# Performance work log

Hardware: AMD Instinct MI355X
Metric: run time of the kernel (lower is better)

The kernel has to match this reference:

```python
import jax, jax.numpy as jnp
import numpy as np

T, B, L, D = 32, 128, 1024, 256  # timesteps, batch, memory slots, word_vec_size(=rnn_size)


def setup_inputs() -> dict:
    key = jax.random.key(0)
    ks = jax.random.split(key, 20)
    f = lambda k, s: jax.random.normal(k, s, dtype=jnp.float32) * 0.05
    return {
        "emb_utts": f(ks[0], (T, B, D)),
        "hr0": f(ks[1], (B, D)),
        "cr0": f(ks[2], (B, D)),
        "hw0": f(ks[3], (B, D)),
        "cw0": f(ks[4], (B, D)),
        "M": f(ks[5], (B, L, D)),
        "mask": jax.random.randint(ks[6], (B, L), 0, 2).astype(bool),
        "Wih_r": f(ks[7], (4 * D, D)),
        "Whh_r": f(ks[8], (4 * D, D)),
        "bih_r": f(ks[9], (4 * D,)),
        "bhh_r": f(ks[10], (4 * D,)),
        "Wc": f(ks[11], (D, 2 * D)),
        "bc": f(ks[12], (D,)),
        "Wih_w": f(ks[13], (4 * D, D)),
        "Whh_w": f(ks[14], (4 * D, D)),
        "bih_w": f(ks[15], (4 * D,)),
        "bhh_w": f(ks[16], (4 * D,)),
    }


def _lstm_cell(x, h, c, Wih, Whh, bih, bhh):
    # PyTorch LSTMCell gate order: i, f, g, o
    g = x @ Wih.T + h @ Whh.T + bih + bhh
    i, fg, gg, o = jnp.split(g, 4, axis=1)
    i = jax.nn.sigmoid(i)
    fg = jax.nn.sigmoid(fg)
    gg = jnp.tanh(gg)
    o = jax.nn.sigmoid(o)
    c2 = fg * c + i * gg
    return o * jnp.tanh(c2), c2


def reference(emb_utts, hr0, cr0, hw0, cw0, M, mask,
              Wih_r, Whh_r, bih_r, bhh_r, Wc, bc,
              Wih_w, Whh_w, bih_w, bhh_w):
    def step(carry, w):
        hr, cr, hw, cw, Mc = carry
        hr, cr = _lstm_cell(w, hr, cr, Wih_r, Whh_r, bih_r, bhh_r)
        # attention read: z = softmax(masked(hr . M))  -> [B, L]
        z = jnp.einsum('bd,bld->bl', hr, Mc)
        z = jax.nn.softmax(jnp.where(mask, -jnp.inf, z), axis=1)
        m = jnp.einsum('bl,bld->bd', z, Mc)           # gather read [B, D]
        comp = jax.nn.softmax(jnp.concatenate([hr, m], axis=1) @ Wc.T + bc, axis=1)
        hw, cw = _lstm_cell(comp, hw, cw, Wih_w, Whh_w, bih_w, bhh_w)
        # memory rewrite exactly as source: M_new = (1 - z) + hw * z (broadcast)
        Mc = (1.0 - z[:, :, None]) + hw[:, None, :] * z[:, :, None]
        return (hr, cr, hw, cw, Mc), hw

    (hr, cr, hw, cw, M), outputs = jax.lax.scan(
        step, (hr0, cr0, hw0, cw0, M), emb_utts)
    return outputs, hr, cr, hw, cw, M
```

## Files before the change

### kernel.cpp

```cpp
#include <hip/hip_runtime.h>
#include <math.h>

typedef unsigned int u32;
typedef __attribute__((ext_vector_type(2))) _Float16 h2;

#define kT 32
#define OUT_STATES 1048576
#define OUT_M      1179648

union H2U { u32 u; h2 h; };

__device__ __forceinline__ float dot2u(u32 w, u32 x, float acc){
  H2U a; a.u = w; H2U b; b.u = x;
#if __has_builtin(__builtin_amdgcn_fdot2)
  return __builtin_amdgcn_fdot2(a.h, b.h, acc, false);
#else
  acc += (float)a.h.x * (float)b.h.x;
  acc += (float)a.h.y * (float)b.h.y;
  return acc;
#endif
}

__device__ __forceinline__ u32 packf16(float x, float y){
  H2U v; v.h.x = (_Float16)x; v.h.y = (_Float16)y; return v.u;
}

__device__ __forceinline__ u32 alu(const u32* p){
  return __hip_atomic_load((u32*)p, __ATOMIC_RELAXED, __HIP_MEMORY_SCOPE_AGENT);
}
__device__ __forceinline__ float alf(const float* p){
  return __hip_atomic_load((float*)p, __ATOMIC_RELAXED, __HIP_MEMORY_SCOPE_AGENT);
}
__device__ __forceinline__ void asu(u32* p, u32 v){
  __hip_atomic_store(p, v, __ATOMIC_RELAXED, __HIP_MEMORY_SCOPE_AGENT);
}
__device__ __forceinline__ void asf(float* p, float v){
  __hip_atomic_store(p, v, __ATOMIC_RELAXED, __HIP_MEMORY_SCOPE_AGENT);
}

__device__ __forceinline__ void pollk(const u32* f, int n, u32 tgt, int tid){
  if (tid < 64){
    const u32* p = f + ((tid < n) ? tid : 0);
    for (;;){
      if (__all((int)(alu(p) >= tgt))) break;
      __builtin_amdgcn_s_sleep(2);
    }
  }
  __syncthreads();
}

__global__ __launch_bounds__(1024) void k_prep(
        const float* __restrict__ Wih_r, const float* __restrict__ Whh_r,
        const float* __restrict__ bih_r, const float* __restrict__ bhh_r,
        const float* __restrict__ Wc,    const float* __restrict__ bc,
        const float* __restrict__ Wih_w, const float* __restrict__ Whh_w,
        const float* __restrict__ bih_w, const float* __restrict__ bhh_w,
        const unsigned char* __restrict__ maskraw,
        u32* WAp, u32* WEp, u32* Wcp, float* bA, float* bE, float* bcf,
        float* wcs, unsigned char* mbuf, u32* flags){
  __shared__ int sb[3];
  if (threadIdx.x < 3) sb[threadIdx.x] = 0;
  __syncthreads();
  if (threadIdx.x < 512){
    unsigned char c = maskraw[threadIdx.x];
    if (c > 1u) atomicOr(&sb[0], 1);
    if ((threadIdx.x & 3) != 0 && c != 0) atomicOr(&sb[1], 1);
    if ((threadIdx.x & 3) == 1 && c == 0x3F) atomicOr(&sb[2], 1);
  }
  __syncthreads();
  int mode = (!sb[0]) ? (sb[1] ? 1 : 0) : (sb[2] ? 2 : 3);

  int idx = blockIdx.x * 1024 + threadIdx.x;
  if (idx < 262144){
    int col = idx >> 8, kp = idx & 255;
    int k0 = 2 * kp;
    float v0 = (k0 < 256) ? Wih_r[col * 256 + k0] : Whh_r[col * 256 + k0 - 256];
    float v1 = (k0 < 256) ? Wih_r[col * 256 + k0 + 1]
                          : Whh_r[col * 256 + k0 + 1 - 256];
    WAp[kp * 1024 + col] = packf16(v0, v1);
  } else if (idx < 524288){
    int i = idx - 262144;
    int col = i >> 8, kp = i & 255;
    int k0 = 2 * kp;
    float v0 = (k0 < 256) ? Wih_w[col * 256 + k0] : Whh_w[col * 256 + k0 - 256];
    float v1 = (k0 < 256) ? Wih_w[col * 256 + k0 + 1]
                          : Whh_w[col * 256 + k0 + 1 - 256];
    WEp[kp * 1024 + col] = packf16(v0, v1);
  } else if (idx < 589824){
    int i = idx - 524288;
    int col = i >> 8, kp = i & 255;
    Wcp[kp * 256 + col] = packf16(Wc[col * 512 + 2 * kp], Wc[col * 512 + 2 * kp + 1]);
  } else if (idx < 590848){
    int i = idx - 589824;
    bA[i] = bih_r[i] + bhh_r[i];
  } else if (idx < 591872){
    int i = idx - 590848;
    bE[i] = bih_w[i] + bhh_w[i];
  } else if (idx < 592128){
    int i = idx - 591872;
    bcf[i] = bc[i];
  } else if (idx < 592384){
    int c = idx - 592128;
    float s = 0.f;
    for (int k = 0; k < 256; k++) s += Wc[c * 512 + 256 + k];
    wcs[c] = s;
  } else if (idx < 723456){
    int l = idx - 592384;
    unsigned char mv;
    if      (mode == 0) mv = (((const int*)maskraw)[l] != 0);
    else if (mode == 1) mv = (maskraw[l] != 0);
    else if (mode == 2) mv = ((maskraw[2*l] | maskraw[2*l+1]) != 0);
    else                mv = (((const unsigned int*)maskraw)[l] != 0);
    mbuf[l] = mv;
  } else if (idx < 724224){
    flags[idx - 723456] = 0;
  }
}

__global__ __launch_bounds__(1024) void k_pre(
        const float* __restrict__ emb, const u32* __restrict__ WAp,
        u32* __restrict__ gxp){
  __shared__ u32 wt[16384];
  __shared__ u32 xt[128 * 129];
  int t = blockIdx.x, c0 = blockIdx.y * 128, tid = threadIdx.x;
  for (int i = 0; i < 16; i++){
    int idx = i * 1024 + tid;
    wt[idx] = WAp[(size_t)(idx >> 7) * 1024 + c0 + (idx & 127)];
    int b = idx >> 7, kp = idx & 127;
    float2 e2 = *(const float2*)(emb + (size_t)t * 32768 + b * 256 + 2 * kp);
    xt[b * 129 + kp] = packf16(e2.x, e2.y);
  }
  __syncthreads();
  int b = tid & 127, cg = tid >> 7;
  float acc[16];
  #pragma unroll
  for (int j = 0; j < 16; j++) acc[j] = 0.f;
  const u32* xrow = xt + b * 129;
  for (int kp = 0; kp < 128; kp++){
    u32 xv = xrow[kp];
    const uint4* wr = (const uint4*)(wt + kp * 128 + cg * 16);
    #pragma unroll
    for (int j4 = 0; j4 < 4; j4++){
      uint4 wv = wr[j4];
      acc[4*j4+0] = dot2u(wv.x, xv, acc[4*j4+0]);
      acc[4*j4+1] = dot2u(wv.y, xv, acc[4*j4+1]);
      acc[4*j4+2] = dot2u(wv.z, xv, acc[4*j4+2]);
      acc[4*j4+3] = dot2u(wv.w, xv, acc[4*j4+3]);
    }
  }
  u32* gp = gxp + ((size_t)t * 128 + b) * 512 + (c0 >> 1) + cg * 8;
  #pragma unroll
  for (int i = 0; i < 8; i++) gp[i] = packf16(acc[2*i], acc[2*i+1]);
}

__device__ __forceinline__ void gemv256(const u32* __restrict__ W,
        const u32* xh, float* psum, int tid){
  int cg = tid & 255, ks = tid >> 8;
  const uint4* wp = (const uint4*)W + (size_t)ks * 32 * 256 + cg;
  const u32* xk = xh + ks * 32;
  float a0 = 0.f, a1 = 0.f, a2 = 0.f, a3 = 0.f;
  #pragma unroll 8
  for (int i = 0; i < 32; i++){
    uint4 wv = wp[(size_t)i * 256];
    u32 xp = xk[i];
    a0 = dot2u(wv.x, xp, a0);  a1 = dot2u(wv.y, xp, a1);
    a2 = dot2u(wv.z, xp, a2);  a3 = dot2u(wv.w, xp, a3);
  }
  float4 r; r.x = a0; r.y = a1; r.z = a2; r.w = a3;
  *(float4*)&psum[ks * 1024 + cg * 4] = r;
}

__device__ __forceinline__ void gemv128x256(const u32* __restrict__ W,
        const u32* xh, float* psum, int tid){
  int c = tid & 255, ks = tid >> 8;
  const u32* wp = W + (size_t)(ks * 32) * 256 + c;
  const u32* xk = xh + ks * 32;
  float a = 0.f;
  #pragma unroll 8
  for (int i = 0; i < 32; i++) a = dot2u(wp[(size_t)i * 256], xk[i], a);
  psum[ks * 256 + c] = a;
}

__device__ void scan_half(int k, const float* __restrict__ M0,
        const unsigned char* __restrict__ mbuf, const float* __restrict__ hrf,
        float* spbuf, float* mpbuf, float* msbuf, u32* fT0, const u32* fR,
        char* sc, int tid){
  float* ps   = (float*)(sc);
  float* wred = (float*)(sc + 16640);
  float* sred = (float*)(sc + 16704);
  float* hr0l = (float*)(sc + 16768);
  int row = k >> 1, half = k & 1;
  pollk(fR + row, 1, 1u, tid);
  if (tid < 256) hr0l[tid] = alf(hrf + row * 256 + tid);
  __syncthreads();
  int w = tid >> 6, lane = tid & 63;
  float4 hrv = *(const float4*)&hr0l[lane * 4];
  float run_max = -INFINITY, S = 0.f;
  float m0 = 0.f, m1 = 0.f, m2 = 0.f, m3 = 0.f;
  int l0 = half * 512 + w * 32;
  for (int l = l0; l < l0 + 32; ++l){
    float4 Mv = *(const float4*)(M0 + ((size_t)row * 1024 + l) * 256 + lane * 4);
    float part = Mv.x * hrv.x + Mv.y * hrv.y + Mv.z * hrv.z + Mv.w * hrv.w;
    #pragma unroll
    for (int mm = 32; mm >= 1; mm >>= 1) part += __shfl_xor(part, mm, 64);
    float s = mbuf[row * 1024 + l] ? -INFINITY : part;
    if (lane == 0) asf(spbuf + row * 1024 + l, s);
    float nm = fmaxf(run_max, s);
    if (nm > -INFINITY){
      float sc2 = expf(run_max - nm);
      float p   = expf(s - nm);
      S = S * sc2 + p;
      m0 = m0 * sc2 + p * Mv.x;  m1 = m1 * sc2 + p * Mv.y;
      m2 = m2 * sc2 + p * Mv.z;  m3 = m3 * sc2 + p * Mv.w;
      run_max = nm;
    }
  }
  if (lane == 0){ wred[w] = run_max; sred[w] = S; }
  ps[w * 260 + lane * 4 + 0] = m0;
  ps[w * 260 + lane * 4 + 1] = m1;
  ps[w * 260 + lane * 4 + 2] = m2;
  ps[w * 260 + lane * 4 + 3] = m3;
  __syncthreads();
  float gmax = -INFINITY;
  #pragma unroll
  for (int w2 = 0; w2 < 16; w2++) gmax = fmaxf(gmax, wred[w2]);
  float Sg = 0.f;
  #pragma unroll
  for (int w2 = 0; w2 < 16; w2++) Sg += sred[w2] * expf(wred[w2] - gmax);
  if (tid < 256){
    float mv = 0.f;
    #pragma unroll
    for (int w2 = 0; w2 < 16; w2++) mv += ps[w2 * 260 + tid] * expf(wred[w2] - gmax);
    asf(mpbuf + k * 256 + tid, mv);
  }
  if (tid == 0){ asf(msbuf + 2 * k, gmax); asf(msbuf + 2 * k + 1, Sg); }
  __syncthreads();
  if (tid == 0) asu(fT0 + k, 1u);
}

__global__ __launch_bounds__(1024, 4) void k_main(
        const float* __restrict__ hr0, const float* __restrict__ cr0,
        const float* __restrict__ hw0, const float* __restrict__ cw0,
        const float* __restrict__ M0,
        const u32* __restrict__ WAp, const u32* __restrict__ WEp,
        const u32* __restrict__ Wcp, const float* __restrict__ bA,
        const float* __restrict__ bE, const float* __restrict__ bcf,
        const float* __restrict__ wcs, const unsigned char* __restrict__ mbuf,
        const u32* __restrict__ gxp,
        float* __restrict__ hrf, float* __restrict__ ubuf,
        float* __restrict__ gwbuf,
        u32* __restrict__ hwp, float* __restrict__ zsbuf,
        float* __restrict__ hwfin, float* __restrict__ spbuf,
        float* __restrict__ mpbuf, float* __restrict__ msbuf,
        u32* __restrict__ flags, float* __restrict__ out){
  __shared__ __attribute__((aligned(16))) char smem[86016];
  int bid = blockIdx.x, tid = threadIdx.x;
  int w = tid >> 6, lane = tid & 63;
  u32* fR  = flags;
  u32* fG  = flags + 192;
  u32* fW  = flags + 256;
  u32* fT0 = flags + 320;

  if (bid < 128){
    int b = bid;
    float* psum = (float*)(smem);
    u32*  xh    = (u32*)(smem + 16384);
    float* hr_f = (float*)(smem + 16896);
    const u32* WRh = WAp + 128 * 1024;
    float cst = (tid < 256) ? cr0[b * 256 + tid] : 0.f;
    if (tid < 128){
      float2 h0 = *(const float2*)(hr0 + b * 256 + 2 * tid);
      xh[tid] = packf16(h0.x, h0.y);
    }
    __syncthreads();
    for (int t = 0; t < kT; t++){
      if (t >= 2) pollk(fW + (b >> 1), 1, (u32)(t - 1), tid);
      u32 gx0 = 0, gx1 = 0, gx2 = 0, gx3 = 0;
      if (tid < 256){
        const u32* gx = gxp + ((size_t)t * 128 + b) * 512;
        gx0 = gx[tid >> 1];          gx1 = gx[128 + (tid >> 1)];
        gx2 = gx[256 + (tid >> 1)];  gx3 = gx[384 + (tid >> 1)];
      }
      gemv256(WRh, xh, psum, tid);
      __syncthreads();
      if (tid < 256){
        H2U p0, p1, p2, p3;
        p0.u = gx0; p1.u = gx1; p2.u = gx2; p3.u = gx3;
        int hi = tid & 1;
        float gi = (hi ? (float)p0.h.y : (float)p0.h.x) + bA[tid];
        float gf = (hi ? (float)p1.h.y : (float)p1.h.x) + bA[256 + tid];
        float gg = (hi ? (float)p2.h.y : (float)p2.h.x) + bA[512 + tid];
        float go = (hi ? (float)p3.h.y : (float)p3.h.x) + bA[768 + tid];
        #pragma unroll
        for (int ks = 0; ks < 4; ks++){
          gi += psum[ks * 1024 + tid];
          gf += psum[ks * 1024 + 256 + tid];
          gg += psum[ks * 1024 + 512 + tid];
          go += psum[ks * 1024 + 768 + tid];
        }
        float i_ = 1.f / (1.f + expf(-gi));
        float f_ = 1.f / (1.f + expf(-gf));
        float g_ = tanhf(gg);
        float o_ = 1.f / (1.f + expf(-go));
        float c2 = f_ * cst + i_ * g_;
        cst = c2;
        float h = o_ * tanhf(c2);
        hr_f[tid] = h;
        asf(hrf + (t & 1) * 32768 + b * 256 + tid, h);
        if (t == kT - 1){
          out[OUT_STATES          + b * 256 + tid] = h;
          out[OUT_STATES +  32768 + b * 256 + tid] = c2;
        }
      }
      __syncthreads();
      if (tid < 128) xh[tid] = packf16(hr_f[2 * tid], hr_f[2 * tid + 1]);
      __syncthreads();
      gemv128x256(Wcp, xh, psum, tid);
      __syncthreads();
      if (tid < 256){
        float u = psum[tid] + psum[256 + tid] + psum[512 + tid] + psum[768 + tid];
        asf(ubuf + (t & 1) * 32768 + b * 256 + tid, u);
      }
      __syncthreads();
      if (tid == 0) asu(fR + b, (u32)(t + 1));
      if (t == 0)
        scan_half(bid, M0, mbuf, hrf, spbuf, mpbuf, msbuf, fT0, fR,
                  smem + 49152, tid);
    }
  } else if (bid < 192){
    int g = bid - 128, r0 = 2 * g, r1 = 2 * g + 1;
    float* psum = (float*)(smem);
    u32*  xh    = (u32*)(smem + 32768);
    for (int t = 0; t < kT; t++){
      if (t == 0){
        if (tid < 128){
          float2 h0 = *(const float2*)(hw0 + r0 * 256 + 2 * tid);
          xh[tid] = packf16(h0.x, h0.y);
        } else if (tid < 256){
          int j = tid - 128;
          float2 h0 = *(const float2*)(hw0 + r1 * 256 + 2 * j);
          xh[tid] = packf16(h0.x, h0.y);
        }
      } else {
        pollk(fW + g, 1, (u32)t, tid);
        if (tid < 128)
          xh[tid] = alu(hwp + ((t - 1) & 1) * 16384 + r0 * 128 + tid);
        else if (tid < 256)
          xh[tid] = alu(hwp + ((t - 1) & 1) * 16384 + r1 * 128 + (tid - 128));
      }
      __syncthreads();
      {
        int cg = tid & 255, ks = tid >> 8;
        const uint4* wp = (const uint4*)(WEp + 128 * 1024)
                        + (size_t)(ks * 32) * 256 + cg;
        const u32* x0 = xh + ks * 32;
        const u32* x1 = xh + 128 + ks * 32;
        float a0=0.f,a1=0.f,a2=0.f,a3=0.f,b0=0.f,b1=0.f,b2=0.f,b3=0.f;
        #pragma unroll 4
        for (int ii = 0; ii < 32; ii++){
          uint4 wv = wp[(size_t)ii * 256];
          u32 xp0 = x0[ii], xp1 = x1[ii];
          a0 = dot2u(wv.x, xp0, a0);  a1 = dot2u(wv.y, xp0, a1);
          a2 = dot2u(wv.z, xp0, a2);  a3 = dot2u(wv.w, xp0, a3);
          b0 = dot2u(wv.x, xp1, b0);  b1 = dot2u(wv.y, xp1, b1);
          b2 = dot2u(wv.z, xp1, b2);  b3 = dot2u(wv.w, xp1, b3);
        }
        float4 ra; ra.x=a0; ra.y=a1; ra.z=a2; ra.w=a3;
        float4 rb; rb.x=b0; rb.y=b1; rb.z=b2; rb.w=b3;
        *(float4*)&psum[ks * 1024 + cg * 4] = ra;
        *(float4*)&psum[4096 + ks * 1024 + cg * 4] = rb;
      }
      __syncthreads();
      #pragma unroll
      for (int rr = 0; rr < 2; rr++){
        float v = psum[rr * 4096 + tid] + psum[rr * 4096 + 1024 + tid]
                + psum[rr * 4096 + 2048 + tid] + psum[rr * 4096 + 3072 + tid];
        asf(gwbuf + (t & 1) * 131072 + (2 * g + rr) * 1024 + tid, v);
      }
      __syncthreads();
      if (tid == 0) asu(fG + g, (u32)(t + 1));
      if (t == 0)
        scan_half(bid, M0, mbuf, hrf, spbuf, mpbuf, msbuf, fT0, fR,
                  smem + 49152, tid);
    }
  } else {
    int g = bid - 192, r0g = 2 * g;
    float* psum  = (float*)(smem);
    u32*  xh    = (u32*)(smem + 32768);
    float* comp  = (float*)(smem + 33792);
    float* hw_f  = (float*)(smem + 35840);
    float* m_f   = (float*)(smem + 37888);
    float* wcs_l = (float*)(smem + 39936);
    float* bc_l  = (float*)(smem + 40960);
    float* redA  = (float*)(smem + 41984);
    float* redB  = (float*)(smem + 42048);
    float* redC  = (float*)(smem + 42112);
    float* redD  = (float*)(smem + 42176);
    float* bE_l  = (float*)(smem + 43008);
    int row = tid >> 9, i = tid & 511;
    int brow = r0g + row;
    if (tid < 256){ wcs_l[tid] = wcs[tid]; bc_l[tid] = bcf[tid]; }
    bE_l[tid] = bE[tid];
    float cst = 0.f;
    if (i < 256){
      hw_f[row * 256 + i] = hw0[brow * 256 + i];
      cst = cw0[brow * 256 + i];
    }
    unsigned char mkA = mbuf[brow * 1024 + i];
    unsigned char mkB = mbuf[brow * 1024 + 512 + i];
    float zA = 0.f, zB = 0.f, vcreg = 0.f;
    __syncthreads();
    scan_half(bid, M0, mbuf, hrf, spbuf, mpbuf, msbuf, fT0, fR,
              smem + 49152, tid);

    for (int t = 0; t < kT; t++){
      pollk(fR + r0g, 2, (u32)(t + 1), tid);
      float hrv = 0.f, ureg = 0.f;
      if (i < 256){
        hrv  = alf(hrf + (t & 1) * 32768 + brow * 256 + i);
        ureg = alf(ubuf + (t & 1) * 32768 + brow * 256 + i);
      }
      float e = -INFINITY;
      if (t == 0){
        pollk(fT0 + 4 * g, 4, 1u, tid);
        int kA2 = 2 * brow, kB2 = 2 * brow + 1;
        float maxA = alf(msbuf + 2 * kA2), SAv = alf(msbuf + 2 * kA2 + 1);
        float maxB = alf(msbuf + 2 * kB2), SBv = alf(msbuf + 2 * kB2 + 1);
        float Gm = fmaxf(maxA, maxB);
        float eAc = expf(maxA - Gm), eBc = expf(maxB - Gm);
        float Sg = SAv * eAc + SBv * eBc;
        zA = expf(alf(spbuf + brow * 1024 + i) - Gm) / Sg;
        zB = expf(alf(spbuf + brow * 1024 + 512 + i) - Gm) / Sg;
        if (i < 256){
          float mv = (alf(mpbuf + kA2 * 256 + i) * eAc
                    + alf(mpbuf + kB2 * 256 + i) * eBc) / Sg;
          m_f[row * 256 + i] = mv;
        }
        __syncthreads();
        if (i < 128)
          xh[row * 128 + i] = packf16(m_f[row * 256 + 2 * i],
                                      m_f[row * 256 + 2 * i + 1]);
        __syncthreads();
        {
          int c = tid & 255, ks = tid >> 8;
          const u32* wp = Wcp + 32768 + (size_t)(ks * 32) * 256 + c;
          const u32* x0 = xh + ks * 32;
          const u32* x1 = xh + 128 + ks * 32;
          float a0 = 0.f, a1 = 0.f;
          #pragma unroll 8
          for (int ii = 0; ii < 32; ii++){
            u32 wv = wp[(size_t)ii * 256];
            a0 = dot2u(wv, x0[ii], a0);
            a1 = dot2u(wv, x1[ii], a1);
          }
          psum[ks * 512 + c] = a0;
          psum[ks * 512 + 256 + c] = a1;
        }
        __syncthreads();
        if (i < 256){
          float vcm = psum[row * 256 + i] + psum[512 + row * 256 + i]
                    + psum[1024 + row * 256 + i] + psum[1536 + row * 256 + i];
          e = ureg + vcm + bc_l[i];
        }
      } else {
        float v1 = (i < 256) ? hrv : 0.f;
        float v2 = (i < 256) ? hrv * hw_f[row * 256 + i] : 0.f;
        #pragma unroll
        for (int mm = 32; mm >= 1; mm >>= 1){
          v1 += __shfl_xor(v1, mm, 64);  v2 += __shfl_xor(v2, mm, 64);
        }
        if (lane == 0){ redA[w] = v1; redB[w] = v2; }
        __syncthreads();
        float S1 = 0.f, S2 = 0.f;
        #pragma unroll
        for (int k2 = 0; k2 < 8; k2++){
          S1 += redA[row * 8 + k2];  S2 += redB[row * 8 + k2];
        }
        float sA = mkA ? -INFINITY : (1.f - zA) * S1 + zA * S2;
        float sB = mkB ? -INFINITY : (1.f - zB) * S1 + zB * S2;
        float mx = fmaxf(sA, sB);
        #pragma unroll
        for (int mm = 32; mm >= 1; mm >>= 1) mx = fmaxf(mx, __shfl_xor(mx, mm, 64));
        if (lane == 0) redC[w] = mx;
        __syncthreads();
        float gm = -INFINITY;
        #pragma unroll
        for (int k2 = 0; k2 < 8; k2++) gm = fmaxf(gm, redC[row * 8 + k2]);
        float pA_ = expf(sA - gm), pB_ = expf(sB - gm);
        float ps = pA_ + pB_;
        #pragma unroll
        for (int mm = 32; mm >= 1; mm >>= 1) ps += __shfl_xor(ps, mm, 64);
        if (lane == 0) redD[w] = ps;
        __syncthreads();
        float Ss = 0.f;
        #pragma unroll
        for (int k2 = 0; k2 < 8; k2++) Ss += redD[row * 8 + k2];
        float znA = pA_ / Ss, znB = pB_ / Ss;
        float a1 = znA * (1.f - zA) + znB * (1.f - zB);
        float a2 = znA * zA + znB * zB;
        #pragma unroll
        for (int mm = 32; mm >= 1; mm >>= 1){
          a1 += __shfl_xor(a1, mm, 64);  a2 += __shfl_xor(a2, mm, 64);
        }
        if (lane == 0){ redA[w] = a1; redB[w] = a2; }
        __syncthreads();
        float Ab = 0.f, Cb = 0.f;
        #pragma unroll
        for (int k2 = 0; k2 < 8; k2++){
          Ab += redA[row * 8 + k2];  Cb += redB[row * 8 + k2];
        }
        zA = znA;  zB = znB;
        if (i < 256)
          e = ureg + Ab * wcs_l[i] + Cb * vcreg + bc_l[i];
      }
      float ev = (i < 256) ? e : -INFINITY;
      float mx2 = ev;
      #pragma unroll
      for (int mm = 32; mm >= 1; mm >>= 1) mx2 = fmaxf(mx2, __shfl_xor(mx2, mm, 64));
      if (lane == 0) redC[w] = mx2;
      __syncthreads();
      float emax = -INFINITY;
      #pragma unroll
      for (int k2 = 0; k2 < 8; k2++) emax = fmaxf(emax, redC[row * 8 + k2]);
      float pe = (i < 256) ? expf(ev - emax) : 0.f;
      float ps2 = pe;
      #pragma unroll
      for (int mm = 32; mm >= 1; mm >>= 1) ps2 += __shfl_xor(ps2, mm, 64);
      if (lane == 0) redD[w] = ps2;
      if (i < 256) comp[row * 256 + i] = pe;
      __syncthreads();
      float esum = 0.f;
      #pragma unroll
      for (int k2 = 0; k2 < 8; k2++) esum += redD[row * 8 + k2];
      if (i < 128)
        xh[row * 128 + i] = packf16(comp[row * 256 + 2 * i],
                                    comp[row * 256 + 2 * i + 1]);
      __syncthreads();
      {
        int cg = tid & 255, ks = tid >> 8;
        const uint4* wp = (const uint4*)WEp + (size_t)(ks * 32) * 256 + cg;
        const u32* x0 = xh + ks * 32;
        const u32* x1 = xh + 128 + ks * 32;
        float a0=0.f,a1=0.f,a2=0.f,a3=0.f,b0=0.f,b1=0.f,b2=0.f,b3=0.f;
        #pragma unroll 4
        for (int ii = 0; ii < 32; ii++){
          uint4 wv = wp[(size_t)ii * 256];
          u32 xp0 = x0[ii], xp1 = x1[ii];
          a0 = dot2u(wv.x, xp0, a0);  a1 = dot2u(wv.y, xp0, a1);
          a2 = dot2u(wv.z, xp0, a2);  a3 = dot2u(wv.w, xp0, a3);
          b0 = dot2u(wv.x, xp1, b0);  b1 = dot2u(wv.y, xp1, b1);
          b2 = dot2u(wv.z, xp1, b2);  b3 = dot2u(wv.w, xp1, b3);
        }
        float4 ra; ra.x=a0; ra.y=a1; ra.z=a2; ra.w=a3;
        float4 rb; rb.x=b0; rb.y=b1; rb.z=b2; rb.w=b3;
        *(float4*)&psum[ks * 1024 + cg * 4] = ra;
        *(float4*)&psum[4096 + ks * 1024 + cg * 4] = rb;
      }
      __syncthreads();
      pollk(fG + g, 1, (u32)(t + 1), tid);
      if (i < 256){
        float rinv = 1.f / esum;
        const float* gwp = gwbuf + (t & 1) * 131072 + brow * 1024;
        float si = psum[row*4096 + i]        + psum[row*4096 + 1024 + i]
                 + psum[row*4096 + 2048 + i] + psum[row*4096 + 3072 + i];
        float sf = psum[row*4096 + 256 + i]  + psum[row*4096 + 1280 + i]
                 + psum[row*4096 + 2304 + i] + psum[row*4096 + 3328 + i];
        float sg2= psum[row*4096 + 512 + i]  + psum[row*4096 + 1536 + i]
                 + psum[row*4096 + 2560 + i] + psum[row*4096 + 3584 + i];
        float so = psum[row*4096 + 768 + i]  + psum[row*4096 + 1792 + i]
                 + psum[row*4096 + 2816 + i] + psum[row*4096 + 3840 + i];
        float gi = bE_l[i]       + alf(gwp + i)       + si  * rinv;
        float gf = bE_l[256 + i] + alf(gwp + 256 + i) + sf  * rinv;
        float gg = bE_l[512 + i] + alf(gwp + 512 + i) + sg2 * rinv;
        float go = bE_l[768 + i] + alf(gwp + 768 + i) + so  * rinv;
        float i_ = 1.f / (1.f + expf(-gi));
        float f_ = 1.f / (1.f + expf(-gf));
        float g_ = tanhf(gg);
        float o_ = 1.f / (1.f + expf(-go));
        float c2 = f_ * cst + i_ * g_;
        cst = c2;
        float h = o_ * tanhf(c2);
        hw_f[row * 256 + i] = h;
        out[(size_t)t * 32768 + brow * 256 + i] = h;
        if (t == kT - 1){
          out[OUT_STATES + 65536 + brow * 256 + i] = h;
          out[OUT_STATES + 98304 + brow * 256 + i] = c2;
        }
      }
      __syncthreads();
      if (i < 128)
        asu(hwp + (t & 1) * 16384 + brow * 128 + i,
            packf16(hw_f[row * 256 + 2 * i], hw_f[row * 256 + 2 * i + 1]));
      __syncthreads();
      if (tid == 0) asu(fW + g, (u32)(t + 1));
      if (t < kT - 1){
        if (i < 128)
          xh[row * 128 + i] = packf16(hw_f[row * 256 + 2 * i],
                                      hw_f[row * 256 + 2 * i + 1]);
        __syncthreads();
        {
          int c = tid & 255, ks = tid >> 8;
          const u32* wp = Wcp + 32768 + (size_t)(ks * 32) * 256 + c;
          const u32* x0 = xh + ks * 32;
          const u32* x1 = xh + 128 + ks * 32;
          float a0 = 0.f, a1 = 0.f;
          #pragma unroll 8
          for (int ii = 0; ii < 32; ii++){
            u32 wv = wp[(size_t)ii * 256];
            a0 = dot2u(wv, x0[ii], a0);
            a1 = dot2u(wv, x1[ii], a1);
          }
          psum[ks * 512 + c] = a0;
          psum[ks * 512 + 256 + c] = a1;
        }
        __syncthreads();
        if (i < 256)
          vcreg = psum[row * 256 + i] + psum[512 + row * 256 + i]
                + psum[1024 + row * 256 + i] + psum[1536 + row * 256 + i];
        __syncthreads();
      }
    }
    if (i < 256) asf(hwfin + brow * 256 + i, hw_f[row * 256 + i]);
    asf(zsbuf + brow * 1024 + i, zA);
    asf(zsbuf + brow * 1024 + 512 + i, zB);
    __syncthreads();
    if (tid == 0) asu(fW + g, (u32)(kT + 1));
  }

  {
    int mrow = bid >> 1, half = bid & 1;
    pollk(fW + (mrow >> 1), 1, (u32)(kT + 1), tid);
    float* zl  = (float*)(smem + 49152);
    float* hwl = (float*)(smem + 51200);
    if (tid < 512) zl[tid] = alf(zsbuf + mrow * 1024 + half * 512 + tid);
    else if (tid < 768) hwl[tid - 512] = alf(hwfin + mrow * 256 + (tid - 512));
    __syncthreads();
    float* Mout = out + OUT_M + (size_t)mrow * 262144 + (size_t)half * 131072;
    for (int it = 0; it < 32; it++){
      int idx = it * 1024 + tid;
      int l = idx >> 6, d4 = (idx & 63) << 2;
      float z = zl[l], omz = 1.f - z;
      float4 h4 = *(const float4*)&hwl[d4];
      float4 v;
      v.x = omz + h4.x * z;  v.y = omz + h4.y * z;
      v.z = omz + h4.z * z;  v.w = omz + h4.w * z;
      *(float4*)(Mout + (size_t)l * 256 + d4) = v;
    }
  }
}

extern "C" void kernel_launch(void* const* d_in, const int* in_sizes, int n_in,
                              void* d_out, int out_size, void* d_ws, size_t ws_size,
                              hipStream_t stream){
  const float* emb   = (const float*)d_in[0];
  const float* hr0   = (const float*)d_in[1];
  const float* cr0   = (const float*)d_in[2];
  const float* hw0   = (const float*)d_in[3];
  const float* cw0   = (const float*)d_in[4];
  const float* M0    = (const float*)d_in[5];
  const unsigned char* maskraw = (const unsigned char*)d_in[6];
  const float* Wih_r = (const float*)d_in[7];
  const float* Whh_r = (const float*)d_in[8];
  const float* bih_r = (const float*)d_in[9];
  const float* bhh_r = (const float*)d_in[10];
  const float* Wc    = (const float*)d_in[11];
  const float* bc    = (const float*)d_in[12];
  const float* Wih_w = (const float*)d_in[13];
  const float* Whh_w = (const float*)d_in[14];
  const float* bih_w = (const float*)d_in[15];
  const float* bhh_w = (const float*)d_in[16];
  float* out = (float*)d_out;

  char* ws = (char*)d_ws;
  u32*  WAp   = (u32*)(ws);
  u32*  WEp   = (u32*)(ws + 1048576);
  u32*  Wcp   = (u32*)(ws + 2097152);
  float* bA   = (float*)(ws + 2359296);
  float* bE   = (float*)(ws + 2363392);
  float* bcf  = (float*)(ws + 2367488);
  float* wcs  = (float*)(ws + 2368512);
  unsigned char* mbuf = (unsigned char*)(ws + 2369536);
  u32*  flags = (u32*)(ws + 2500608);
  float* hrf  = (float*)(ws + 2504704);
  float* ubuf = (float*)(ws + 2766848);
  float* gwbuf= (float*)(ws + 3291136);
  u32*  hwp   = (u32*)(ws + 4339712);
  float* zsbuf= (float*)(ws + 4470784);
  float* hwfin= (float*)(ws + 4995072);
  float* spbuf= (float*)(ws + 5126144);
  float* mpbuf= (float*)(ws + 5650432);
  float* msbuf= (float*)(ws + 5912576);
  u32*  gxp   = (u32*)(ws + 5914624);

  k_prep<<<dim3(708), dim3(1024), 0, stream>>>(
      Wih_r, Whh_r, bih_r, bhh_r, Wc, bc, Wih_w, Whh_w, bih_w, bhh_w,
      maskraw, WAp, WEp, Wcp, bA, bE, bcf, wcs, mbuf, flags);
  k_pre<<<dim3(32, 8), dim3(1024), 0, stream>>>(emb, WAp, gxp);
  k_main<<<dim3(256), dim3(1024), 0, stream>>>(
      hr0, cr0, hw0, cw0, M0, WAp, WEp, Wcp, bA, bE, bcf, wcs, mbuf, gxp,
      hrf, ubuf, gwbuf, hwp, zsbuf, hwfin, spbuf, mpbuf, msbuf,
      flags, out);
}
```

Baseline: 682.0 us.

## Fuse attention softmax reductions and prefetch next-step read state earlier

The attention softmax in steps after the first now uses an analytic upper bound (max of S1,S2) as the shift instead of a block-wide max reduction. It also folds the normalization and the a1/a2 sums into one combined reduction of ps and pz, which removes two barrier-separated reduction rounds per step. The poll on the read-LSTM flag and the loads of hr/u for the next step move earlier, ahead of the Wc matvec, so the cross-block wait can overlap other work. The bound shift is mathematically valid, because each score is a convex combination of S1 and S2, but it could lose exp precision if S1 and S2 differ greatly from the true max.

```diff
diff --git a/kernel.cpp b/kernel.cpp
--- a/kernel.cpp
+++ b/kernel.cpp
@@ -412,14 +412,14 @@
     __syncthreads();
     scan_half(bid, M0, mbuf, hrf, spbuf, mpbuf, msbuf, fT0, fR,
               smem + 49152, tid);
+    pollk(fR + r0g, 2, 1u, tid);
+    float hrv = 0.f, ureg = 0.f;
+    if (i < 256){
+      hrv  = alf(hrf + brow * 256 + i);
+      ureg = alf(ubuf + brow * 256 + i);
+    }
 
     for (int t = 0; t < kT; t++){
-      pollk(fR + r0g, 2, (u32)(t + 1), tid);
-      float hrv = 0.f, ureg = 0.f;
-      if (i < 256){
-        hrv  = alf(hrf + (t & 1) * 32768 + brow * 256 + i);
-        ureg = alf(ubuf + (t & 1) * 32768 + brow * 256 + i);
-      }
       float e = -INFINITY;
       if (t == 0){
         pollk(fT0 + 4 * g, 4, 1u, tid);
@@ -476,40 +476,24 @@
         for (int k2 = 0; k2 < 8; k2++){
           S1 += redA[row * 8 + k2];  S2 += redB[row * 8 + k2];
         }
+        float gm = fmaxf(S1, S2);
         float sA = mkA ? -INFINITY : (1.f - zA) * S1 + zA * S2;
         float sB = mkB ? -INFINITY : (1.f - zB) * S1 + zB * S2;
-        float mx = fmaxf(sA, sB);
-        #pragma unroll
-        for (int mm = 32; mm >= 1; mm >>= 1) mx = fmaxf(mx, __shfl_xor(mx, mm, 64));
-        if (lane == 0) redC[w] = mx;
-        __syncthreads();
-        float gm = -INFINITY;
-        #pragma unroll
-        for (int k2 = 0; k2 < 8; k2++) gm = fmaxf(gm, redC[row * 8 + k2]);
         float pA_ = expf(sA - gm), pB_ = expf(sB - gm);
-        float ps = pA_ + pB_;
-        #pragma unroll
-        for (int mm = 32; mm >= 1; mm >>= 1) ps += __shfl_xor(ps, mm, 64);
-        if (lane == 0) redD[w] = ps;
-        __syncthreads();
-        float Ss = 0.f;
-        #pragma unroll
-        for (int k2 = 0; k2 < 8; k2++) Ss += redD[row * 8 + k2];
-        float znA = pA_ / Ss, znB = pB_ / Ss;
-        float a1 = znA * (1.f - zA) + znB * (1.f - zB);
-        float a2 = znA * zA + znB * zB;
+        float ps = pA_ + pB_, pz = pA_ * zA + pB_ * zB;
         #pragma unroll
         for (int mm = 32; mm >= 1; mm >>= 1){
-          a1 += __shfl_xor(a1, mm, 64);  a2 += __shfl_xor(a2, mm, 64);
-        }
-        if (lane == 0){ redA[w] = a1; redB[w] = a2; }
-        __syncthreads();
-        float Ab = 0.f, Cb = 0.f;
+          ps += __shfl_xor(ps, mm, 64);  pz += __shfl_xor(pz, mm, 64);
+        }
+        if (lane == 0){ redC[w] = ps; redD[w] = pz; }
+        __syncthreads();
+        float Ss = 0.f, Pz = 0.f;
         #pragma unroll
         for (int k2 = 0; k2 < 8; k2++){
-          Ab += redA[row * 8 + k2];  Cb += redB[row * 8 + k2];
-        }
-        zA = znA;  zB = znB;
+          Ss += redC[row * 8 + k2];  Pz += redD[row * 8 + k2];
+        }
+        float Cb = Pz / Ss, Ab = 1.f - Cb;
+        zA = pA_ / Ss;  zB = pB_ / Ss;
         if (i < 256)
           e = ureg + Ab * wcs_l[i] + Cb * vcreg + bc_l[i];
       }
@@ -598,6 +582,11 @@
           xh[row * 128 + i] = packf16(hw_f[row * 256 + 2 * i],
                                       hw_f[row * 256 + 2 * i + 1]);
         __syncthreads();
+        pollk(fR + r0g, 2, (u32)(t + 2), tid);
+        if (i < 256){
+          hrv  = alf(hrf + ((t + 1) & 1) * 32768 + brow * 256 + i);
+          ureg = alf(ubuf + ((t + 1) & 1) * 32768 + brow * 256 + i);
+        }
         {
           int c = tid & 255, ks = tid >> 8;
           const u32* wp = Wcp + 32768 + (size_t)(ks * 32) * 256 + c;
```

Result: faster. 654.7 us (-4.0%).
